# Kernel tuning notes

Measured on AMD Instinct MI355X. Metric: run time of the kernel, lower is better.

## Reference

```python
import jax, jax.numpy as jnp
import numpy as np

N_NODES = 100000
N_EDGES = 3200000
EMBED_DIM = 64
BATCH = 16384


def setup_inputs() -> dict:
    key = jax.random.key(0)
    k1, k2, k3, k4 = jax.random.split(key, 4)
    gcn_weight = jax.random.normal(k1, (N_NODES, EMBED_DIM), dtype=jnp.float32) * 0.1
    gcn_bias = jnp.zeros((EMBED_DIM,), dtype=jnp.float32)
    linear_weight = jax.random.normal(k2, (N_NODES, 1), dtype=jnp.float32) * 0.1
    linear_bias = jnp.zeros((1,), dtype=jnp.float32)
    edge_index = jax.random.randint(k3, (2, N_EDGES), 0, N_NODES, dtype=jnp.int64)
    interaction_pairs = jax.random.randint(k4, (BATCH, 2), 0, N_NODES, dtype=jnp.int64)
    return {
        "gcn_weight": gcn_weight,
        "gcn_bias": gcn_bias,
        "linear_weight": linear_weight,
        "linear_bias": linear_bias,
        "edge_index": edge_index,
        "interaction_pairs": interaction_pairs,
    }


def _gcn_conv_identity_features(gcn_weight, gcn_bias, edge_index):
    # Features X = I, so X @ W = W. GCNConv output = D^{-1/2}(A+I)D^{-1/2} W + b.
    src, dst = edge_index[0], edge_index[1]
    ones = jnp.ones((src.shape[0],), dtype=gcn_weight.dtype)
    # degree (with self loop) computed on destination nodes, as in PyG gcn_norm
    deg = jax.ops.segment_sum(ones, dst, num_segments=N_NODES) + 1.0
    dinv = jax.lax.rsqrt(deg)  # [N]
    norm = dinv[src] * dinv[dst]  # [E]
    msg = gcn_weight[src] * norm[:, None]  # [E, D] -- dominant memory traffic
    agg = jax.ops.segment_sum(msg, dst, num_segments=N_NODES)  # [N, D]
    # self-loop term: norm_ii = 1/deg[i]
    out = agg + gcn_weight * (dinv * dinv)[:, None] + gcn_bias
    return out


def reference(gcn_weight, gcn_bias, linear_weight, linear_bias, edge_index, interaction_pairs):
    node_emb = _gcn_conv_identity_features(gcn_weight, gcn_bias, edge_index)  # [N, D]
    e = node_emb[interaction_pairs]  # [B, 2, D] gather
    # FM pairwise interaction: 0.5 * sum_d ((sum_f e)^2 - sum_f e^2)
    sum_sq = jnp.square(jnp.sum(e, axis=1))  # [B, D]
    sq_sum = jnp.sum(jnp.square(e), axis=1)  # [B, D]
    fm = 0.5 * jnp.sum(sum_sq - sq_sum, axis=1, keepdims=True)  # [B, 1]
    # FeaturesLinear: sum of per-node scalar embeddings + bias
    lin = jnp.sum(linear_weight[interaction_pairs], axis=1) + linear_bias  # [B, 1]
    return jnp.squeeze(lin + fm, axis=1)  # [B]
```

## Files before the change

### kernel.cpp

```cpp
#include <hip/hip_runtime.h>

#define N_NODES 100000
#define N_EDGES 3200000
#define BATCH 16384
#define MAX_SLOTS 32768

#define NW 12500
#define SLICES 256
#define EPS2 12500
#define I4PS2 3125

#define NBUCK 256
#define BCAP 8192
#define BCAP_SH 13
#define EBCAP 4608

#define OFF_SLOT      0
#define OFF_DINV      400000
#define OFF_NODELIST  800000
#define OFF_GCUR      931072
#define OFF_PARTIALS  932096
#define OFF_WH        13732096
#define OFF_BINS      26532096
#define OFF_EMB       34920704

__device__ __forceinline__ unsigned bfr(float f) {
    unsigned u = __float_as_uint(f);
    return (u + 0x7FFFu + ((u >> 16) & 1u)) >> 16;
}
__device__ __forceinline__ float bfx(unsigned h) {
    return __uint_as_float(h << 16);
}

__global__ void k_flags(const int* __restrict__ pairs, unsigned* __restrict__ slot,
                        int* __restrict__ nodelist, unsigned* __restrict__ gcur) {
    int i = blockIdx.x * blockDim.x + threadIdx.x;
    if (i < NBUCK) gcur[i] = (unsigned)(i << BCAP_SH);
    if (i < 2 * BATCH) {
        int n = pairs[i];
        nodelist[i] = n;
        slot[n] = (unsigned)(i + 1);
    }
}

__device__ __forceinline__ int cert(int d, const unsigned* __restrict__ slot,
                                    const int* __restrict__ nodelist) {
    unsigned r = slot[d];
    unsigned idx = r - 1u;
    if (idx < (unsigned)MAX_SLOTS && nodelist[idx] == d) return (int)idx;
    return -1;
}

__global__ void k_hist(const int* __restrict__ src, const int* __restrict__ dst,
                       const unsigned* __restrict__ slot, const int* __restrict__ nodelist,
                       unsigned* __restrict__ partials, unsigned* __restrict__ gcur,
                       unsigned* __restrict__ bins) {
    __shared__ unsigned h[NW];
    __shared__ unsigned ebuf[EBCAP];
    __shared__ int lc[NBUCK];
    __shared__ int base[NBUCK];
    __shared__ int ecnt;
    int g = blockIdx.x;
    int tid = threadIdx.x;
    int lane = tid & 63;
    for (int i = tid; i < NW; i += 512) h[i] = 0;
    if (tid < NBUCK) lc[tid] = 0;
    if (tid == 0) ecnt = 0;
    __syncthreads();
    const int4* d4 = (const int4*)(dst + g * EPS2);
    const int4* s4 = (const int4*)(src + g * EPS2);
    for (int i = tid; i < I4PS2; i += 512) {
        int4 v = d4[i];
        int4 s = s4[i];
        atomicAdd(&h[v.x >> 3], 1u << ((v.x & 7) << 2));
        atomicAdd(&h[v.y >> 3], 1u << ((v.y & 7) << 2));
        atomicAdd(&h[v.z >> 3], 1u << ((v.z & 7) << 2));
        atomicAdd(&h[v.w >> 3], 1u << ((v.w & 7) << 2));
#define STAGE(dc, sc)                                                          \
        {                                                                      \
            int t = cert(dc, slot, nodelist);                                  \
            unsigned long long mk = __ballot(t >= 0);                          \
            int bs = 0;                                                        \
            if (lane == 0) bs = atomicAdd(&ecnt, (int)__popcll(mk));           \
            bs = __shfl(bs, 0, 64);                                            \
            if (t >= 0) {                                                      \
                int off = bs + (int)__popcll(mk & ((1ull << lane) - 1ull));    \
                if (off < EBCAP) {                                             \
                    ebuf[off] = ((unsigned)t << 17) | (unsigned)(sc);          \
                    atomicAdd(&lc[t >> 7], 1);                                 \
                }                                                              \
            }                                                                  \
        }
        STAGE(v.x, s.x)
        STAGE(v.y, s.y)
        STAGE(v.z, s.z)
        STAGE(v.w, s.w)
#undef STAGE
    }
    __syncthreads();
    unsigned* outp = partials + (unsigned)g * NW;
    for (int i = tid; i < NW; i += 512) outp[i] = h[i];
    if (tid < NBUCK) {
        base[tid] = (int)atomicAdd(&gcur[tid], (unsigned)lc[tid]);
        lc[tid] = 0;
    }
    __syncthreads();
    int ne = ecnt;
    if (ne > EBCAP) ne = EBCAP;
    for (int j = tid; j < ne; j += 512) {
        unsigned e = ebuf[j];
        int b = (int)(e >> 24);
        int r = atomicAdd(&lc[b], 1);
        unsigned pos = (unsigned)base[b] + (unsigned)r;
        if (pos < (unsigned)((b + 1) << BCAP_SH)) bins[pos] = e;
    }
}

__global__ void k_mid(const unsigned* __restrict__ partials, const float4* __restrict__ w4,
                      float* __restrict__ dinv, uint4* __restrict__ wh4) {
    __shared__ unsigned pA[256], pB[256], pC[256], pD[256];
    __shared__ float sdinv[256];
    int blk = blockIdx.x;
    int wi = threadIdx.x & 31, sg = threadIdx.x >> 5;
    int w = blk * 32 + wi;
    unsigned A = 0, B = 0, C = 0, D = 0;
    if (w < NW) {
        const unsigned* q = partials + w;
#pragma unroll
        for (int ch = 0; ch < 2; ++ch) {
            unsigned x = 0, y = 0;
#pragma unroll
            for (int k = 0; k < 16; ++k) {
                unsigned v = q[(unsigned)(sg * 32 + ch * 16 + k) * NW];
                x += v & 0x0F0F0F0Fu;
                y += (v >> 4) & 0x0F0F0F0Fu;
            }
            A += x & 0x00FF00FFu;
            B += (x >> 8) & 0x00FF00FFu;
            C += y & 0x00FF00FFu;
            D += (y >> 8) & 0x00FF00FFu;
        }
    }
    pA[threadIdx.x] = A; pB[threadIdx.x] = B; pC[threadIdx.x] = C; pD[threadIdx.x] = D;
    __syncthreads();
    if (threadIdx.x < 32 && w < NW) {
        unsigned sA = 0, sB = 0, sC = 0, sD = 0;
#pragma unroll
        for (int k = 0; k < 8; ++k) {
            sA += pA[k * 32 + wi]; sB += pB[k * 32 + wi];
            sC += pC[k * 32 + wi]; sD += pD[k * 32 + wi];
        }
        float4 d0, d1;
        d0.x = rsqrtf((float)(sA & 0xFFFFu) + 1.0f);
        d0.y = rsqrtf((float)(sC & 0xFFFFu) + 1.0f);
        d0.z = rsqrtf((float)(sB & 0xFFFFu) + 1.0f);
        d0.w = rsqrtf((float)(sD & 0xFFFFu) + 1.0f);
        d1.x = rsqrtf((float)(sA >> 16) + 1.0f);
        d1.y = rsqrtf((float)(sC >> 16) + 1.0f);
        d1.z = rsqrtf((float)(sB >> 16) + 1.0f);
        d1.w = rsqrtf((float)(sD >> 16) + 1.0f);
        ((float4*)dinv)[w * 2] = d0;
        ((float4*)dinv)[w * 2 + 1] = d1;
        int lb = wi * 8;
        sdinv[lb + 0] = d0.x; sdinv[lb + 1] = d0.y; sdinv[lb + 2] = d0.z; sdinv[lb + 3] = d0.w;
        sdinv[lb + 4] = d1.x; sdinv[lb + 5] = d1.y; sdinv[lb + 6] = d1.z; sdinv[lb + 7] = d1.w;
    }
    __syncthreads();
#pragma unroll
    for (int it = 0; it < 8; ++it) {
        int k = blk * 2048 + it * 256 + threadIdx.x;
        if (k < N_NODES * 8) {
            float4 va = w4[k * 2];
            float4 vb = w4[k * 2 + 1];
            float d = sdinv[(k >> 3) - blk * 256];
            uint4 o;
            o.x = bfr(va.x * d) | (bfr(va.y * d) << 16);
            o.y = bfr(va.z * d) | (bfr(va.w * d) << 16);
            o.z = bfr(vb.x * d) | (bfr(vb.y * d) << 16);
            o.w = bfr(vb.z * d) | (bfr(vb.w * d) << 16);
            wh4[k] = o;
        }
    }
}

__global__ void k_gfuse(const unsigned* __restrict__ gcur, const unsigned* __restrict__ bins,
                        const int* __restrict__ nodelist, const uint4* __restrict__ wh4,
                        const float* __restrict__ dinv, const float4* __restrict__ bias4,
                        uint4* __restrict__ emb4) {
    __shared__ unsigned ebuf2[BCAP];
    __shared__ int lc[128], st[128];
    int b = blockIdx.x >> 2;
    int qt = blockIdx.x & 3;
    int tid = threadIdx.x;
    int cnt = (int)(gcur[b] - (unsigned)(b << BCAP_SH));
    if (cnt > BCAP) cnt = BCAP;
    const unsigned* bp = bins + ((unsigned)b << BCAP_SH);
    if (tid < 128) lc[tid] = 0;
    __syncthreads();
    for (int j = tid; j < cnt; j += 512) atomicAdd(&lc[(bp[j] >> 17) & 127], 1);
    __syncthreads();
    if (tid < 128) st[tid] = lc[tid];
    __syncthreads();
    for (int off = 1; off < 128; off <<= 1) {
        int v = (tid < 128 && tid >= off) ? st[tid - off] : 0;
        __syncthreads();
        if (tid < 128) st[tid] += v;
        __syncthreads();
    }
    if (tid < 128) {
        st[tid] -= lc[tid];
        lc[tid] = st[tid];
    }
    __syncthreads();
    for (int j = tid; j < cnt; j += 512) {
        unsigned e = bp[j];
        int r = atomicAdd(&lc[(e >> 17) & 127], 1);
        ebuf2[r] = e & 0x1FFFFu;
    }
    __syncthreads();
    int wave = tid >> 6, lane = tid & 63;
    int rg = lane >> 3, dp = lane & 7;
#pragma unroll
    for (int q = 0; q < 4; ++q) {
        int sl = qt * 32 + wave * 4 + q;
        int s0 = st[sl];
        int cn = lc[sl] - s0;
        double a0 = 0., a1 = 0., a2 = 0., a3 = 0., a4 = 0., a5 = 0., a6 = 0., a7 = 0.;
        int j = 0;
        for (; j + 16 <= cn; j += 16) {
            int e0 = (int)ebuf2[s0 + j + rg];
            int e1 = (int)ebuf2[s0 + j + 8 + rg];
            uint4 oa = wh4[(e0 << 3) + dp];
            uint4 ob = wh4[(e1 << 3) + dp];
            a0 += (double)(bfx(oa.x) + bfx(ob.x));
            a1 += (double)(bfx(oa.x >> 16) + bfx(ob.x >> 16));
            a2 += (double)(bfx(oa.y) + bfx(ob.y));
            a3 += (double)(bfx(oa.y >> 16) + bfx(ob.y >> 16));
            a4 += (double)(bfx(oa.z) + bfx(ob.z));
            a5 += (double)(bfx(oa.z >> 16) + bfx(ob.z >> 16));
            a6 += (double)(bfx(oa.w) + bfx(ob.w));
            a7 += (double)(bfx(oa.w >> 16) + bfx(ob.w >> 16));
        }
        for (; j < cn; j += 8) {
            if (rg < cn - j) {
                int e0 = (int)ebuf2[s0 + j + rg];
                uint4 oa = wh4[(e0 << 3) + dp];
                a0 += (double)bfx(oa.x); a1 += (double)bfx(oa.x >> 16);
                a2 += (double)bfx(oa.y); a3 += (double)bfx(oa.y >> 16);
                a4 += (double)bfx(oa.z); a5 += (double)bfx(oa.z >> 16);
                a6 += (double)bfx(oa.w); a7 += (double)bfx(oa.w >> 16);
            }
        }
#pragma unroll
        for (int m = 8; m <= 32; m <<= 1) {
            a0 += __shfl_xor(a0, m, 64); a1 += __shfl_xor(a1, m, 64);
            a2 += __shfl_xor(a2, m, 64); a3 += __shfl_xor(a3, m, 64);
            a4 += __shfl_xor(a4, m, 64); a5 += __shfl_xor(a5, m, 64);
            a6 += __shfl_xor(a6, m, 64); a7 += __shfl_xor(a7, m, 64);
        }
        if (rg == 0) {
            int gslot = (b << 7) + sl;
            int n = nodelist[gslot];
            float dn = dinv[n];
            uint4 u = wh4[(n << 3) + dp];
            float4 b0 = bias4[dp * 2], b1 = bias4[dp * 2 + 1];
            float r0 = ((float)a0 + bfx(u.x)) * dn + b0.x;
            float r1 = ((float)a1 + bfx(u.x >> 16)) * dn + b0.y;
            float r2 = ((float)a2 + bfx(u.y)) * dn + b0.z;
            float r3 = ((float)a3 + bfx(u.y >> 16)) * dn + b0.w;
            float r4 = ((float)a4 + bfx(u.z)) * dn + b1.x;
            float r5 = ((float)a5 + bfx(u.z >> 16)) * dn + b1.y;
            float r6 = ((float)a6 + bfx(u.w)) * dn + b1.z;
            float r7 = ((float)a7 + bfx(u.w >> 16)) * dn + b1.w;
            uint4 o;
            o.x = bfr(r0) | (bfr(r1) << 16);
            o.y = bfr(r2) | (bfr(r3) << 16);
            o.z = bfr(r4) | (bfr(r5) << 16);
            o.w = bfr(r6) | (bfr(r7) << 16);
            emb4[(gslot << 3) + dp] = o;
        }
    }
}

__global__ void k_final(const int* __restrict__ pairs, const unsigned* __restrict__ slot,
                        const uint2* __restrict__ emb2, const float* __restrict__ lw,
                        const float* __restrict__ lb, float* __restrict__ out) {
    int p = (blockIdx.x * blockDim.x + threadIdx.x) >> 4;
    int li = threadIdx.x & 15;
    if (p >= BATCH) return;
    int a = pairs[p * 2], b = pairs[p * 2 + 1];
    int sa = (int)slot[a] - 1;
    int sb = (int)slot[b] - 1;
    uint2 ua = emb2[(sa << 4) + li];
    uint2 ub = emb2[(sb << 4) + li];
    float prod = bfx(ua.x) * bfx(ub.x) + bfx(ua.x >> 16) * bfx(ub.x >> 16)
               + bfx(ua.y) * bfx(ub.y) + bfx(ua.y >> 16) * bfx(ub.y >> 16);
#pragma unroll
    for (int m = 1; m <= 8; m <<= 1) prod += __shfl_xor(prod, m, 64);
    if (li == 0) out[p] = lw[a] + lw[b] + lb[0] + prod;
}

extern "C" void kernel_launch(void* const* d_in, const int* in_sizes, int n_in,
                              void* d_out, int out_size, void* d_ws, size_t ws_size,
                              hipStream_t stream) {
    const float* gcn_weight    = (const float*)d_in[0];
    const float* gcn_bias      = (const float*)d_in[1];
    const float* linear_weight = (const float*)d_in[2];
    const float* linear_bias   = (const float*)d_in[3];
    const int*   edge_index    = (const int*)d_in[4];
    const int*   pairs         = (const int*)d_in[5];
    float* out = (float*)d_out;

    char* ws = (char*)d_ws;
    unsigned* slot      = (unsigned*)(ws + OFF_SLOT);
    float*    dinv      = (float*)   (ws + OFF_DINV);
    int*      nodelist  = (int*)     (ws + OFF_NODELIST);
    unsigned* gcur      = (unsigned*)(ws + OFF_GCUR);
    unsigned* partials  = (unsigned*)(ws + OFF_PARTIALS);
    uint4*    wh4       = (uint4*)   (ws + OFF_WH);
    unsigned* bins      = (unsigned*)(ws + OFF_BINS);
    uint4*    emb4      = (uint4*)   (ws + OFF_EMB);
    uint2*    emb2      = (uint2*)   (ws + OFF_EMB);

    const int* src_arr = edge_index;
    const int* dst_arr = edge_index + N_EDGES;

    k_flags<<<64, 512, 0, stream>>>(pairs, slot, nodelist, gcur);
    k_hist<<<SLICES, 512, 0, stream>>>(src_arr, dst_arr, slot, nodelist,
                                       partials, gcur, bins);
    k_mid<<<391, 256, 0, stream>>>(partials, (const float4*)gcn_weight, dinv, wh4);
    k_gfuse<<<NBUCK * 4, 512, 0, stream>>>(gcur, bins, nodelist, wh4,
                                           dinv, (const float4*)gcn_bias, emb4);
    k_final<<<1024, 256, 0, stream>>>(pairs, slot, emb2, linear_weight, linear_bias, out);
}
```

Measured before the change: 163.1 us.

## Fuse pipeline into single cooperative kernel with grid-wide syncs

Replaces the five separate kernel launches with one cooperative kernel of 256 blocks that uses grid.sync between phases. The bf16 conversion of the weights moves into the histogram phase, and source-node dinv scaling is applied per edge during aggregation rather than folded into the bf16 weights beforehand. The goal is to remove launch gaps and overlap the weight conversion with the histogram work. In exchange it adds grid barriers and an extra dinv gather per edge, and cuts the gather phase to 256 blocks from the earlier 1024.

```diff
diff --git a/kernel.cpp b/kernel.cpp
--- a/kernel.cpp
+++ b/kernel.cpp
@@ -1,4 +1,7 @@
 #include <hip/hip_runtime.h>
+#include <hip/hip_cooperative_groups.h>
+
+namespace cg = cooperative_groups;
 
 #define N_NODES 100000
 #define N_EDGES 3200000
@@ -14,6 +17,10 @@
 #define BCAP 8192
 #define BCAP_SH 13
 #define EBCAP 4608
+
+#define NTHREADS 512
+#define NBLOCKS 256
+#define GSIZE (NTHREADS * NBLOCKS)
 
 #define OFF_SLOT      0
 #define OFF_DINV      400000
@@ -32,17 +39,6 @@
     return __uint_as_float(h << 16);
 }
 
-__global__ void k_flags(const int* __restrict__ pairs, unsigned* __restrict__ slot,
-                        int* __restrict__ nodelist, unsigned* __restrict__ gcur) {
-    int i = blockIdx.x * blockDim.x + threadIdx.x;
-    if (i < NBUCK) gcur[i] = (unsigned)(i << BCAP_SH);
-    if (i < 2 * BATCH) {
-        int n = pairs[i];
-        nodelist[i] = n;
-        slot[n] = (unsigned)(i + 1);
-    }
-}
-
 __device__ __forceinline__ int cert(int d, const unsigned* __restrict__ slot,
                                     const int* __restrict__ nodelist) {
     unsigned r = slot[d];
@@ -51,253 +47,273 @@
     return -1;
 }
 
-__global__ void k_hist(const int* __restrict__ src, const int* __restrict__ dst,
-                       const unsigned* __restrict__ slot, const int* __restrict__ nodelist,
-                       unsigned* __restrict__ partials, unsigned* __restrict__ gcur,
-                       unsigned* __restrict__ bins) {
-    __shared__ unsigned h[NW];
-    __shared__ unsigned ebuf[EBCAP];
-    __shared__ int lc[NBUCK];
-    __shared__ int base[NBUCK];
-    __shared__ int ecnt;
-    int g = blockIdx.x;
-    int tid = threadIdx.x;
-    int lane = tid & 63;
-    for (int i = tid; i < NW; i += 512) h[i] = 0;
-    if (tid < NBUCK) lc[tid] = 0;
-    if (tid == 0) ecnt = 0;
-    __syncthreads();
-    const int4* d4 = (const int4*)(dst + g * EPS2);
-    const int4* s4 = (const int4*)(src + g * EPS2);
-    for (int i = tid; i < I4PS2; i += 512) {
-        int4 v = d4[i];
-        int4 s = s4[i];
-        atomicAdd(&h[v.x >> 3], 1u << ((v.x & 7) << 2));
-        atomicAdd(&h[v.y >> 3], 1u << ((v.y & 7) << 2));
-        atomicAdd(&h[v.z >> 3], 1u << ((v.z & 7) << 2));
-        atomicAdd(&h[v.w >> 3], 1u << ((v.w & 7) << 2));
+union SharedU {
+    struct { unsigned h[NW]; unsigned ebuf[EBCAP]; int lc[NBUCK]; int base[NBUCK]; int ecnt; } p1;
+    struct { unsigned pA[NTHREADS], pB[NTHREADS], pC[NTHREADS], pD[NTHREADS]; } p2;
+    struct { unsigned ebuf2[BCAP]; int lc[128]; int st[128]; } p3;
+};
+
+__global__ void __launch_bounds__(NTHREADS, 1)
+k_mega(const int* __restrict__ pairs, unsigned* __restrict__ slot,
+       int* __restrict__ nodelist, unsigned* __restrict__ gcur,
+       const int* __restrict__ src, const int* __restrict__ dst,
+       unsigned* __restrict__ partials, unsigned* __restrict__ bins,
+       const float4* __restrict__ w4, float* __restrict__ dinv,
+       uint4* __restrict__ wh4, const float4* __restrict__ bias4,
+       uint4* __restrict__ emb4, const float* __restrict__ lw,
+       const float* __restrict__ lb, float* __restrict__ out) {
+    __shared__ SharedU su;
+    cg::grid_group grid = cg::this_grid();
+    const int tid = threadIdx.x;
+    const int gtid = blockIdx.x * NTHREADS + tid;
+    const int lane = tid & 63;
+
+    if (gtid < NBUCK) gcur[gtid] = (unsigned)(gtid << BCAP_SH);
+    if (gtid < 2 * BATCH) {
+        int n = pairs[gtid];
+        nodelist[gtid] = n;
+        slot[n] = (unsigned)(gtid + 1);
+    }
+    __threadfence();
+    grid.sync();
+
+    {
+        int g = blockIdx.x;
+        for (int i = tid; i < NW; i += NTHREADS) su.p1.h[i] = 0;
+        if (tid < NBUCK) su.p1.lc[tid] = 0;
+        if (tid == 0) su.p1.ecnt = 0;
+        __syncthreads();
+        const int4* d4 = (const int4*)(dst + g * EPS2);
+        const int4* s4 = (const int4*)(src + g * EPS2);
+        for (int i = tid; i < I4PS2; i += NTHREADS) {
+            int4 v = d4[i];
+            int4 s = s4[i];
+            atomicAdd(&su.p1.h[v.x >> 3], 1u << ((v.x & 7) << 2));
+            atomicAdd(&su.p1.h[v.y >> 3], 1u << ((v.y & 7) << 2));
+            atomicAdd(&su.p1.h[v.z >> 3], 1u << ((v.z & 7) << 2));
+            atomicAdd(&su.p1.h[v.w >> 3], 1u << ((v.w & 7) << 2));
 #define STAGE(dc, sc)                                                          \
-        {                                                                      \
-            int t = cert(dc, slot, nodelist);                                  \
-            unsigned long long mk = __ballot(t >= 0);                          \
-            int bs = 0;                                                        \
-            if (lane == 0) bs = atomicAdd(&ecnt, (int)__popcll(mk));           \
-            bs = __shfl(bs, 0, 64);                                            \
-            if (t >= 0) {                                                      \
-                int off = bs + (int)__popcll(mk & ((1ull << lane) - 1ull));    \
-                if (off < EBCAP) {                                             \
-                    ebuf[off] = ((unsigned)t << 17) | (unsigned)(sc);          \
-                    atomicAdd(&lc[t >> 7], 1);                                 \
+            {                                                                  \
+                int t = cert(dc, slot, nodelist);                              \
+                unsigned long long mk = __ballot(t >= 0);                      \
+                int bs = 0;                                                    \
+                if (lane == 0) bs = atomicAdd(&su.p1.ecnt, (int)__popcll(mk)); \
+                bs = __shfl(bs, 0, 64);                                        \
+                if (t >= 0) {                                                  \
+                    int off = bs + (int)__popcll(mk & ((1ull << lane) - 1ull));\
+                    if (off < EBCAP) {                                         \
+                        su.p1.ebuf[off] = ((unsigned)t << 17) | (unsigned)(sc);\
+                        atomicAdd(&su.p1.lc[t >> 7], 1);                       \
+                    }                                                          \
                 }                                                              \
-            }                                                                  \
-        }
-        STAGE(v.x, s.x)
-        STAGE(v.y, s.y)
-        STAGE(v.z, s.z)
-        STAGE(v.w, s.w)
+            }
+            STAGE(v.x, s.x)
+            STAGE(v.y, s.y)
+            STAGE(v.z, s.z)
+            STAGE(v.w, s.w)
 #undef STAGE
-    }
-    __syncthreads();
-    unsigned* outp = partials + (unsigned)g * NW;
-    for (int i = tid; i < NW; i += 512) outp[i] = h[i];
-    if (tid < NBUCK) {
-        base[tid] = (int)atomicAdd(&gcur[tid], (unsigned)lc[tid]);
-        lc[tid] = 0;
-    }
-    __syncthreads();
-    int ne = ecnt;
-    if (ne > EBCAP) ne = EBCAP;
-    for (int j = tid; j < ne; j += 512) {
-        unsigned e = ebuf[j];
-        int b = (int)(e >> 24);
-        int r = atomicAdd(&lc[b], 1);
-        unsigned pos = (unsigned)base[b] + (unsigned)r;
-        if (pos < (unsigned)((b + 1) << BCAP_SH)) bins[pos] = e;
-    }
-}
-
-__global__ void k_mid(const unsigned* __restrict__ partials, const float4* __restrict__ w4,
-                      float* __restrict__ dinv, uint4* __restrict__ wh4) {
-    __shared__ unsigned pA[256], pB[256], pC[256], pD[256];
-    __shared__ float sdinv[256];
-    int blk = blockIdx.x;
-    int wi = threadIdx.x & 31, sg = threadIdx.x >> 5;
-    int w = blk * 32 + wi;
-    unsigned A = 0, B = 0, C = 0, D = 0;
-    if (w < NW) {
-        const unsigned* q = partials + w;
-#pragma unroll
-        for (int ch = 0; ch < 2; ++ch) {
-            unsigned x = 0, y = 0;
-#pragma unroll
-            for (int k = 0; k < 16; ++k) {
-                unsigned v = q[(unsigned)(sg * 32 + ch * 16 + k) * NW];
-                x += v & 0x0F0F0F0Fu;
-                y += (v >> 4) & 0x0F0F0F0Fu;
-            }
-            A += x & 0x00FF00FFu;
-            B += (x >> 8) & 0x00FF00FFu;
-            C += y & 0x00FF00FFu;
-            D += (y >> 8) & 0x00FF00FFu;
-        }
-    }
-    pA[threadIdx.x] = A; pB[threadIdx.x] = B; pC[threadIdx.x] = C; pD[threadIdx.x] = D;
-    __syncthreads();
-    if (threadIdx.x < 32 && w < NW) {
-        unsigned sA = 0, sB = 0, sC = 0, sD = 0;
-#pragma unroll
-        for (int k = 0; k < 8; ++k) {
-            sA += pA[k * 32 + wi]; sB += pB[k * 32 + wi];
-            sC += pC[k * 32 + wi]; sD += pD[k * 32 + wi];
-        }
-        float4 d0, d1;
-        d0.x = rsqrtf((float)(sA & 0xFFFFu) + 1.0f);
-        d0.y = rsqrtf((float)(sC & 0xFFFFu) + 1.0f);
-        d0.z = rsqrtf((float)(sB & 0xFFFFu) + 1.0f);
-        d0.w = rsqrtf((float)(sD & 0xFFFFu) + 1.0f);
-        d1.x = rsqrtf((float)(sA >> 16) + 1.0f);
-        d1.y = rsqrtf((float)(sC >> 16) + 1.0f);
-        d1.z = rsqrtf((float)(sB >> 16) + 1.0f);
-        d1.w = rsqrtf((float)(sD >> 16) + 1.0f);
-        ((float4*)dinv)[w * 2] = d0;
-        ((float4*)dinv)[w * 2 + 1] = d1;
-        int lb = wi * 8;
-        sdinv[lb + 0] = d0.x; sdinv[lb + 1] = d0.y; sdinv[lb + 2] = d0.z; sdinv[lb + 3] = d0.w;
-        sdinv[lb + 4] = d1.x; sdinv[lb + 5] = d1.y; sdinv[lb + 6] = d1.z; sdinv[lb + 7] = d1.w;
-    }
-    __syncthreads();
-#pragma unroll
-    for (int it = 0; it < 8; ++it) {
-        int k = blk * 2048 + it * 256 + threadIdx.x;
-        if (k < N_NODES * 8) {
+        }
+        __syncthreads();
+        unsigned* outp = partials + (unsigned)g * NW;
+        for (int i = tid; i < NW; i += NTHREADS) outp[i] = su.p1.h[i];
+        if (tid < NBUCK) {
+            su.p1.base[tid] = (int)atomicAdd(&gcur[tid], (unsigned)su.p1.lc[tid]);
+            su.p1.lc[tid] = 0;
+        }
+        __syncthreads();
+        int ne = su.p1.ecnt;
+        if (ne > EBCAP) ne = EBCAP;
+        for (int j = tid; j < ne; j += NTHREADS) {
+            unsigned e = su.p1.ebuf[j];
+            int b = (int)(e >> 24);
+            int r = atomicAdd(&su.p1.lc[b], 1);
+            unsigned pos = (unsigned)su.p1.base[b] + (unsigned)r;
+            if (pos < (unsigned)((b + 1) << BCAP_SH)) bins[pos] = e;
+        }
+        for (int k = gtid; k < N_NODES * 8; k += GSIZE) {
             float4 va = w4[k * 2];
             float4 vb = w4[k * 2 + 1];
-            float d = sdinv[(k >> 3) - blk * 256];
             uint4 o;
-            o.x = bfr(va.x * d) | (bfr(va.y * d) << 16);
-            o.y = bfr(va.z * d) | (bfr(va.w * d) << 16);
-            o.z = bfr(vb.x * d) | (bfr(vb.y * d) << 16);
-            o.w = bfr(vb.z * d) | (bfr(vb.w * d) << 16);
+            o.x = bfr(va.x) | (bfr(va.y) << 16);
+            o.y = bfr(va.z) | (bfr(va.w) << 16);
+            o.z = bfr(vb.x) | (bfr(vb.y) << 16);
+            o.w = bfr(vb.z) | (bfr(vb.w) << 16);
             wh4[k] = o;
         }
     }
-}
-
-__global__ void k_gfuse(const unsigned* __restrict__ gcur, const unsigned* __restrict__ bins,
-                        const int* __restrict__ nodelist, const uint4* __restrict__ wh4,
-                        const float* __restrict__ dinv, const float4* __restrict__ bias4,
-                        uint4* __restrict__ emb4) {
-    __shared__ unsigned ebuf2[BCAP];
-    __shared__ int lc[128], st[128];
-    int b = blockIdx.x >> 2;
-    int qt = blockIdx.x & 3;
-    int tid = threadIdx.x;
-    int cnt = (int)(gcur[b] - (unsigned)(b << BCAP_SH));
-    if (cnt > BCAP) cnt = BCAP;
-    const unsigned* bp = bins + ((unsigned)b << BCAP_SH);
-    if (tid < 128) lc[tid] = 0;
-    __syncthreads();
-    for (int j = tid; j < cnt; j += 512) atomicAdd(&lc[(bp[j] >> 17) & 127], 1);
-    __syncthreads();
-    if (tid < 128) st[tid] = lc[tid];
-    __syncthreads();
-    for (int off = 1; off < 128; off <<= 1) {
-        int v = (tid < 128 && tid >= off) ? st[tid - off] : 0;
-        __syncthreads();
-        if (tid < 128) st[tid] += v;
-        __syncthreads();
-    }
-    if (tid < 128) {
-        st[tid] -= lc[tid];
-        lc[tid] = st[tid];
-    }
-    __syncthreads();
-    for (int j = tid; j < cnt; j += 512) {
-        unsigned e = bp[j];
-        int r = atomicAdd(&lc[(e >> 17) & 127], 1);
-        ebuf2[r] = e & 0x1FFFFu;
-    }
-    __syncthreads();
-    int wave = tid >> 6, lane = tid & 63;
-    int rg = lane >> 3, dp = lane & 7;
-#pragma unroll
-    for (int q = 0; q < 4; ++q) {
-        int sl = qt * 32 + wave * 4 + q;
-        int s0 = st[sl];
-        int cn = lc[sl] - s0;
-        double a0 = 0., a1 = 0., a2 = 0., a3 = 0., a4 = 0., a5 = 0., a6 = 0., a7 = 0.;
-        int j = 0;
-        for (; j + 16 <= cn; j += 16) {
-            int e0 = (int)ebuf2[s0 + j + rg];
-            int e1 = (int)ebuf2[s0 + j + 8 + rg];
-            uint4 oa = wh4[(e0 << 3) + dp];
-            uint4 ob = wh4[(e1 << 3) + dp];
-            a0 += (double)(bfx(oa.x) + bfx(ob.x));
-            a1 += (double)(bfx(oa.x >> 16) + bfx(ob.x >> 16));
-            a2 += (double)(bfx(oa.y) + bfx(ob.y));
-            a3 += (double)(bfx(oa.y >> 16) + bfx(ob.y >> 16));
-            a4 += (double)(bfx(oa.z) + bfx(ob.z));
-            a5 += (double)(bfx(oa.z >> 16) + bfx(ob.z >> 16));
-            a6 += (double)(bfx(oa.w) + bfx(ob.w));
-            a7 += (double)(bfx(oa.w >> 16) + bfx(ob.w >> 16));
-        }
-        for (; j < cn; j += 8) {
-            if (rg < cn - j) {
-                int e0 = (int)ebuf2[s0 + j + rg];
+    __threadfence();
+    grid.sync();
+
+    {
+        int vb = blockIdx.x;
+        if (vb < 196) {
+            int wi = tid & 63, sg = tid >> 6;
+            int w = vb * 64 + wi;
+            unsigned A = 0, B = 0, C = 0, D = 0;
+            if (w < NW) {
+                const unsigned* q = partials + w;
+#pragma unroll
+                for (int ch = 0; ch < 2; ++ch) {
+                    unsigned x = 0, y = 0;
+#pragma unroll
+                    for (int k = 0; k < 16; ++k) {
+                        unsigned v = q[(unsigned)(sg * 32 + ch * 16 + k) * NW];
+                        x += v & 0x0F0F0F0Fu;
+                        y += (v >> 4) & 0x0F0F0F0Fu;
+                    }
+                    A += x & 0x00FF00FFu;
+                    B += (x >> 8) & 0x00FF00FFu;
+                    C += y & 0x00FF00FFu;
+                    D += (y >> 8) & 0x00FF00FFu;
+                }
+            }
+            su.p2.pA[tid] = A; su.p2.pB[tid] = B; su.p2.pC[tid] = C; su.p2.pD[tid] = D;
+            __syncthreads();
+            if (tid < 64 && w < NW) {
+                unsigned sA = 0, sB = 0, sC = 0, sD = 0;
+#pragma unroll
+                for (int k = 0; k < 8; ++k) {
+                    sA += su.p2.pA[k * 64 + tid]; sB += su.p2.pB[k * 64 + tid];
+                    sC += su.p2.pC[k * 64 + tid]; sD += su.p2.pD[k * 64 + tid];
+                }
+                float4 d0, d1;
+                d0.x = rsqrtf((float)(sA & 0xFFFFu) + 1.0f);
+                d0.y = rsqrtf((float)(sC & 0xFFFFu) + 1.0f);
+                d0.z = rsqrtf((float)(sB & 0xFFFFu) + 1.0f);
+                d0.w = rsqrtf((float)(sD & 0xFFFFu) + 1.0f);
+                d1.x = rsqrtf((float)(sA >> 16) + 1.0f);
+                d1.y = rsqrtf((float)(sC >> 16) + 1.0f);
+                d1.z = rsqrtf((float)(sB >> 16) + 1.0f);
+                d1.w = rsqrtf((float)(sD >> 16) + 1.0f);
+                ((float4*)dinv)[w * 2] = d0;
+                ((float4*)dinv)[w * 2 + 1] = d1;
+            }
+        }
+    }
+    __threadfence();
+    grid.sync();
+
+    {
+        int b = blockIdx.x;
+        int cnt = (int)(gcur[b] - (unsigned)(b << BCAP_SH));
+        if (cnt > BCAP) cnt = BCAP;
+        const unsigned* bp = bins + ((unsigned)b << BCAP_SH);
+        if (tid < 128) su.p3.lc[tid] = 0;
+        __syncthreads();
+        for (int j = tid; j < cnt; j += NTHREADS)
+            atomicAdd(&su.p3.lc[(bp[j] >> 17) & 127], 1);
+        __syncthreads();
+        if (tid < 128) su.p3.st[tid] = su.p3.lc[tid];
+        __syncthreads();
+        for (int off = 1; off < 128; off <<= 1) {
+            int v = (tid < 128 && tid >= off) ? su.p3.st[tid - off] : 0;
+            __syncthreads();
+            if (tid < 128) su.p3.st[tid] += v;
+            __syncthreads();
+        }
+        if (tid < 128) {
+            su.p3.st[tid] -= su.p3.lc[tid];
+            su.p3.lc[tid] = su.p3.st[tid];
+        }
+        __syncthreads();
+        for (int j = tid; j < cnt; j += NTHREADS) {
+            unsigned e = bp[j];
+            int r = atomicAdd(&su.p3.lc[(e >> 17) & 127], 1);
+            su.p3.ebuf2[r] = e & 0x1FFFFu;
+        }
+        __syncthreads();
+        int wave = tid >> 6;
+        int rg = lane >> 3, dp = lane & 7;
+#pragma unroll 1
+        for (int q = 0; q < 16; ++q) {
+            int sl = wave * 16 + q;
+            int s0 = su.p3.st[sl];
+            int cn = su.p3.lc[sl] - s0;
+            double a0 = 0., a1 = 0., a2 = 0., a3 = 0., a4 = 0., a5 = 0., a6 = 0., a7 = 0.;
+            int j = 0;
+            for (; j + 16 <= cn; j += 16) {
+                int e0 = (int)su.p3.ebuf2[s0 + j + rg];
+                int e1 = (int)su.p3.ebuf2[s0 + j + 8 + rg];
+                float dv0 = dinv[e0], dv1 = dinv[e1];
                 uint4 oa = wh4[(e0 << 3) + dp];
-                a0 += (double)bfx(oa.x); a1 += (double)bfx(oa.x >> 16);
-                a2 += (double)bfx(oa.y); a3 += (double)bfx(oa.y >> 16);
-                a4 += (double)bfx(oa.z); a5 += (double)bfx(oa.z >> 16);
-                a6 += (double)bfx(oa.w); a7 += (double)bfx(oa.w >> 16);
-            }
-        }
-#pragma unroll
-        for (int m = 8; m <= 32; m <<= 1) {
-            a0 += __shfl_xor(a0, m, 64); a1 += __shfl_xor(a1, m, 64);
-            a2 += __shfl_xor(a2, m, 64); a3 += __shfl_xor(a3, m, 64);
-            a4 += __shfl_xor(a4, m, 64); a5 += __shfl_xor(a5, m, 64);
-            a6 += __shfl_xor(a6, m, 64); a7 += __shfl_xor(a7, m, 64);
-        }
-        if (rg == 0) {
-            int gslot = (b << 7) + sl;
-            int n = nodelist[gslot];
-            float dn = dinv[n];
-            uint4 u = wh4[(n << 3) + dp];
-            float4 b0 = bias4[dp * 2], b1 = bias4[dp * 2 + 1];
-            float r0 = ((float)a0 + bfx(u.x)) * dn + b0.x;
-            float r1 = ((float)a1 + bfx(u.x >> 16)) * dn + b0.y;
-            float r2 = ((float)a2 + bfx(u.y)) * dn + b0.z;
-            float r3 = ((float)a3 + bfx(u.y >> 16)) * dn + b0.w;
-            float r4 = ((float)a4 + bfx(u.z)) * dn + b1.x;
-            float r5 = ((float)a5 + bfx(u.z >> 16)) * dn + b1.y;
-            float r6 = ((float)a6 + bfx(u.w)) * dn + b1.z;
-            float r7 = ((float)a7 + bfx(u.w >> 16)) * dn + b1.w;
-            uint4 o;
-            o.x = bfr(r0) | (bfr(r1) << 16);
-            o.y = bfr(r2) | (bfr(r3) << 16);
-            o.z = bfr(r4) | (bfr(r5) << 16);
-            o.w = bfr(r6) | (bfr(r7) << 16);
-            emb4[(gslot << 3) + dp] = o;
-        }
-    }
-}
-
-__global__ void k_final(const int* __restrict__ pairs, const unsigned* __restrict__ slot,
-                        const uint2* __restrict__ emb2, const float* __restrict__ lw,
-                        const float* __restrict__ lb, float* __restrict__ out) {
-    int p = (blockIdx.x * blockDim.x + threadIdx.x) >> 4;
-    int li = threadIdx.x & 15;
-    if (p >= BATCH) return;
-    int a = pairs[p * 2], b = pairs[p * 2 + 1];
-    int sa = (int)slot[a] - 1;
-    int sb = (int)slot[b] - 1;
-    uint2 ua = emb2[(sa << 4) + li];
-    uint2 ub = emb2[(sb << 4) + li];
-    float prod = bfx(ua.x) * bfx(ub.x) + bfx(ua.x >> 16) * bfx(ub.x >> 16)
-               + bfx(ua.y) * bfx(ub.y) + bfx(ua.y >> 16) * bfx(ub.y >> 16);
-#pragma unroll
-    for (int m = 1; m <= 8; m <<= 1) prod += __shfl_xor(prod, m, 64);
-    if (li == 0) out[p] = lw[a] + lw[b] + lb[0] + prod;
+                uint4 ob = wh4[(e1 << 3) + dp];
+                a0 += (double)(bfx(oa.x) * dv0 + bfx(ob.x) * dv1);
+                a1 += (double)(bfx(oa.x >> 16) * dv0 + bfx(ob.x >> 16) * dv1);
+                a2 += (double)(bfx(oa.y) * dv0 + bfx(ob.y) * dv1);
+                a3 += (double)(bfx(oa.y >> 16) * dv0 + bfx(ob.y >> 16) * dv1);
+                a4 += (double)(bfx(oa.z) * dv0 + bfx(ob.z) * dv1);
+                a5 += (double)(bfx(oa.z >> 16) * dv0 + bfx(ob.z >> 16) * dv1);
+                a6 += (double)(bfx(oa.w) * dv0 + bfx(ob.w) * dv1);
+                a7 += (double)(bfx(oa.w >> 16) * dv0 + bfx(ob.w >> 16) * dv1);
+            }
+            for (; j < cn; j += 8) {
+                if (rg < cn - j) {
+                    int e0 = (int)su.p3.ebuf2[s0 + j + rg];
+                    float dv0 = dinv[e0];
+                    uint4 oa = wh4[(e0 << 3) + dp];
+                    a0 += (double)(bfx(oa.x) * dv0);
+                    a1 += (double)(bfx(oa.x >> 16) * dv0);
+                    a2 += (double)(bfx(oa.y) * dv0);
+                    a3 += (double)(bfx(oa.y >> 16) * dv0);
+                    a4 += (double)(bfx(oa.z) * dv0);
+                    a5 += (double)(bfx(oa.z >> 16) * dv0);
+                    a6 += (double)(bfx(oa.w) * dv0);
+                    a7 += (double)(bfx(oa.w >> 16) * dv0);
+                }
+            }
+#pragma unroll
+            for (int m = 8; m <= 32; m <<= 1) {
+                a0 += __shfl_xor(a0, m, 64); a1 += __shfl_xor(a1, m, 64);
+                a2 += __shfl_xor(a2, m, 64); a3 += __shfl_xor(a3, m, 64);
+                a4 += __shfl_xor(a4, m, 64); a5 += __shfl_xor(a5, m, 64);
+                a6 += __shfl_xor(a6, m, 64); a7 += __shfl_xor(a7, m, 64);
+            }
+            if (rg == 0) {
+                int gslot = (b << 7) + sl;
+                int n = nodelist[gslot];
+                float dn = dinv[n];
+                uint4 u = wh4[(n << 3) + dp];
+                float4 b0 = bias4[dp * 2], b1 = bias4[dp * 2 + 1];
+                float r0 = ((float)a0 + bfx(u.x) * dn) * dn + b0.x;
+                float r1 = ((float)a1 + bfx(u.x >> 16) * dn) * dn + b0.y;
+                float r2 = ((float)a2 + bfx(u.y) * dn) * dn + b0.z;
+                float r3 = ((float)a3 + bfx(u.y >> 16) * dn) * dn + b0.w;
+                float r4 = ((float)a4 + bfx(u.z) * dn) * dn + b1.x;
+                float r5 = ((float)a5 + bfx(u.z >> 16) * dn) * dn + b1.y;
+                float r6 = ((float)a6 + bfx(u.w) * dn) * dn + b1.z;
+                float r7 = ((float)a7 + bfx(u.w >> 16) * dn) * dn + b1.w;
+                uint4 o;
+                o.x = bfr(r0) | (bfr(r1) << 16);
+                o.y = bfr(r2) | (bfr(r3) << 16);
+                o.z = bfr(r4) | (bfr(r5) << 16);
+                o.w = bfr(r6) | (bfr(r7) << 16);
+                emb4[(gslot << 3) + dp] = o;
+            }
+        }
+    }
+    __threadfence();
+    grid.sync();
+
+    {
+        const uint2* emb2 = (const uint2*)emb4;
+        int li = tid & 15;
+#pragma unroll
+        for (int pass = 0; pass < 2; ++pass) {
+            int p = pass * (GSIZE / 16) + (gtid >> 4);
+            if (p < BATCH) {
+                int a = pairs[p * 2], b = pairs[p * 2 + 1];
+                int sa = (int)slot[a] - 1;
+                int sb = (int)slot[b] - 1;
+                uint2 ua = emb2[(sa << 4) + li];
+                uint2 ub = emb2[(sb << 4) + li];
+                float prod = bfx(ua.x) * bfx(ub.x) + bfx(ua.x >> 16) * bfx(ub.x >> 16)
+                           + bfx(ua.y) * bfx(ub.y) + bfx(ua.y >> 16) * bfx(ub.y >> 16);
+#pragma unroll
+                for (int m = 1; m <= 8; m <<= 1) prod += __shfl_xor(prod, m, 64);
+                if (li == 0) out[p] = lw[a] + lw[b] + lb[0] + prod;
+            }
+        }
+    }
 }
 
 extern "C" void kernel_launch(void* const* d_in, const int* in_sizes, int n_in,
@@ -308,7 +324,7 @@
     const float* linear_weight = (const float*)d_in[2];
     const float* linear_bias   = (const float*)d_in[3];
     const int*   edge_index    = (const int*)d_in[4];
-    const int*   pairs         = (const int*)d_in[5];
+    const int*   pairs_p       = (const int*)d_in[5];
     float* out = (float*)d_out;
 
     char* ws = (char*)d_ws;
@@ -320,16 +336,18 @@
     uint4*    wh4       = (uint4*)   (ws + OFF_WH);
     unsigned* bins      = (unsigned*)(ws + OFF_BINS);
     uint4*    emb4      = (uint4*)   (ws + OFF_EMB);
-    uint2*    emb2      = (uint2*)   (ws + OFF_EMB);
 
     const int* src_arr = edge_index;
     const int* dst_arr = edge_index + N_EDGES;
-
-    k_flags<<<64, 512, 0, stream>>>(pairs, slot, nodelist, gcur);
-    k_hist<<<SLICES, 512, 0, stream>>>(src_arr, dst_arr, slot, nodelist,
-                                       partials, gcur, bins);
-    k_mid<<<391, 256, 0, stream>>>(partials, (const float4*)gcn_weight, dinv, wh4);
-    k_gfuse<<<NBUCK * 4, 512, 0, stream>>>(gcur, bins, nodelist, wh4,
-                                           dinv, (const float4*)gcn_bias, emb4);
-    k_final<<<1024, 256, 0, stream>>>(pairs, slot, emb2, linear_weight, linear_bias, out);
-}
+    const float4* w4f   = (const float4*)gcn_weight;
+    const float4* bias4 = (const float4*)gcn_bias;
+
+    void* args[] = {
+        (void*)&pairs_p, (void*)&slot, (void*)&nodelist, (void*)&gcur,
+        (void*)&src_arr, (void*)&dst_arr, (void*)&partials, (void*)&bins,
+        (void*)&w4f, (void*)&dinv, (void*)&wh4, (void*)&bias4,
+        (void*)&emb4, (void*)&linear_weight, (void*)&linear_bias, (void*)&out
+    };
+    hipLaunchCooperativeKernel((const void*)k_mega, dim3(NBLOCKS), dim3(NTHREADS),
+                               args, 0, stream);
+}
```

Result: slower. 497.6 us (+205.0%).

## Move bf16 weight conversion into histogram kernel and apply dinv at gather

Applied to the files above, without the earlier changes.

The fp32-to-bf16 conversion of the GCN weight table moves out of k_mid and into the tail of k_hist, with no dinv scaling applied there. The gather kernel now loads dinv[src] per edge and multiplies it in, and applies dn to the self-loop term as well. This leaves k_mid as a small degree-reduction kernel. k_hist and k_gfuse move to 1024-thread blocks, and k_gfuse uses half as many blocks with its q loop no longer unrolled. The cost is an extra random 4-byte dinv load per edge in the gather, and the conversion now sits on k_hist's critical path.

```diff
diff --git a/kernel.cpp b/kernel.cpp
--- a/kernel.cpp
+++ b/kernel.cpp
@@ -14,6 +14,9 @@
 #define BCAP 8192
 #define BCAP_SH 13
 #define EBCAP 4608
+
+#define HIST_THREADS 1024
+#define HGSIZE (SLICES * HIST_THREADS)
 
 #define OFF_SLOT      0
 #define OFF_DINV      400000
@@ -54,7 +57,8 @@
 __global__ void k_hist(const int* __restrict__ src, const int* __restrict__ dst,
                        const unsigned* __restrict__ slot, const int* __restrict__ nodelist,
                        unsigned* __restrict__ partials, unsigned* __restrict__ gcur,
-                       unsigned* __restrict__ bins) {
+                       unsigned* __restrict__ bins,
+                       const float4* __restrict__ w4, uint4* __restrict__ wh4) {
     __shared__ unsigned h[NW];
     __shared__ unsigned ebuf[EBCAP];
     __shared__ int lc[NBUCK];
@@ -63,13 +67,13 @@
     int g = blockIdx.x;
     int tid = threadIdx.x;
     int lane = tid & 63;
-    for (int i = tid; i < NW; i += 512) h[i] = 0;
+    for (int i = tid; i < NW; i += HIST_THREADS) h[i] = 0;
     if (tid < NBUCK) lc[tid] = 0;
     if (tid == 0) ecnt = 0;
     __syncthreads();
     const int4* d4 = (const int4*)(dst + g * EPS2);
     const int4* s4 = (const int4*)(src + g * EPS2);
-    for (int i = tid; i < I4PS2; i += 512) {
+    for (int i = tid; i < I4PS2; i += HIST_THREADS) {
         int4 v = d4[i];
         int4 s = s4[i];
         atomicAdd(&h[v.x >> 3], 1u << ((v.x & 7) << 2));
@@ -99,7 +103,7 @@
     }
     __syncthreads();
     unsigned* outp = partials + (unsigned)g * NW;
-    for (int i = tid; i < NW; i += 512) outp[i] = h[i];
+    for (int i = tid; i < NW; i += HIST_THREADS) outp[i] = h[i];
     if (tid < NBUCK) {
         base[tid] = (int)atomicAdd(&gcur[tid], (unsigned)lc[tid]);
         lc[tid] = 0;
@@ -107,19 +111,27 @@
     __syncthreads();
     int ne = ecnt;
     if (ne > EBCAP) ne = EBCAP;
-    for (int j = tid; j < ne; j += 512) {
+    for (int j = tid; j < ne; j += HIST_THREADS) {
         unsigned e = ebuf[j];
         int b = (int)(e >> 24);
         int r = atomicAdd(&lc[b], 1);
         unsigned pos = (unsigned)base[b] + (unsigned)r;
         if (pos < (unsigned)((b + 1) << BCAP_SH)) bins[pos] = e;
     }
-}
-
-__global__ void k_mid(const unsigned* __restrict__ partials, const float4* __restrict__ w4,
-                      float* __restrict__ dinv, uint4* __restrict__ wh4) {
+    for (int k = g * HIST_THREADS + tid; k < N_NODES * 8; k += HGSIZE) {
+        float4 va = w4[k * 2];
+        float4 vb = w4[k * 2 + 1];
+        uint4 o;
+        o.x = bfr(va.x) | (bfr(va.y) << 16);
+        o.y = bfr(va.z) | (bfr(va.w) << 16);
+        o.z = bfr(vb.x) | (bfr(vb.y) << 16);
+        o.w = bfr(vb.z) | (bfr(vb.w) << 16);
+        wh4[k] = o;
+    }
+}
+
+__global__ void k_mid(const unsigned* __restrict__ partials, float* __restrict__ dinv) {
     __shared__ unsigned pA[256], pB[256], pC[256], pD[256];
-    __shared__ float sdinv[256];
     int blk = blockIdx.x;
     int wi = threadIdx.x & 31, sg = threadIdx.x >> 5;
     int w = blk * 32 + wi;
@@ -161,25 +173,6 @@
         d1.w = rsqrtf((float)(sD >> 16) + 1.0f);
         ((float4*)dinv)[w * 2] = d0;
         ((float4*)dinv)[w * 2 + 1] = d1;
-        int lb = wi * 8;
-        sdinv[lb + 0] = d0.x; sdinv[lb + 1] = d0.y; sdinv[lb + 2] = d0.z; sdinv[lb + 3] = d0.w;
-        sdinv[lb + 4] = d1.x; sdinv[lb + 5] = d1.y; sdinv[lb + 6] = d1.z; sdinv[lb + 7] = d1.w;
-    }
-    __syncthreads();
-#pragma unroll
-    for (int it = 0; it < 8; ++it) {
-        int k = blk * 2048 + it * 256 + threadIdx.x;
-        if (k < N_NODES * 8) {
-            float4 va = w4[k * 2];
-            float4 vb = w4[k * 2 + 1];
-            float d = sdinv[(k >> 3) - blk * 256];
-            uint4 o;
-            o.x = bfr(va.x * d) | (bfr(va.y * d) << 16);
-            o.y = bfr(va.z * d) | (bfr(va.w * d) << 16);
-            o.z = bfr(vb.x * d) | (bfr(vb.y * d) << 16);
-            o.w = bfr(vb.z * d) | (bfr(vb.w * d) << 16);
-            wh4[k] = o;
-        }
     }
 }
 
@@ -189,15 +182,15 @@
                         uint4* __restrict__ emb4) {
     __shared__ unsigned ebuf2[BCAP];
     __shared__ int lc[128], st[128];
-    int b = blockIdx.x >> 2;
-    int qt = blockIdx.x & 3;
+    int b = blockIdx.x >> 1;
+    int half = blockIdx.x & 1;
     int tid = threadIdx.x;
     int cnt = (int)(gcur[b] - (unsigned)(b << BCAP_SH));
     if (cnt > BCAP) cnt = BCAP;
     const unsigned* bp = bins + ((unsigned)b << BCAP_SH);
     if (tid < 128) lc[tid] = 0;
     __syncthreads();
-    for (int j = tid; j < cnt; j += 512) atomicAdd(&lc[(bp[j] >> 17) & 127], 1);
+    for (int j = tid; j < cnt; j += 1024) atomicAdd(&lc[(bp[j] >> 17) & 127], 1);
     __syncthreads();
     if (tid < 128) st[tid] = lc[tid];
     __syncthreads();
@@ -212,7 +205,7 @@
         lc[tid] = st[tid];
     }
     __syncthreads();
-    for (int j = tid; j < cnt; j += 512) {
+    for (int j = tid; j < cnt; j += 1024) {
         unsigned e = bp[j];
         int r = atomicAdd(&lc[(e >> 17) & 127], 1);
         ebuf2[r] = e & 0x1FFFFu;
@@ -220,9 +213,9 @@
     __syncthreads();
     int wave = tid >> 6, lane = tid & 63;
     int rg = lane >> 3, dp = lane & 7;
-#pragma unroll
+#pragma unroll 1
     for (int q = 0; q < 4; ++q) {
-        int sl = qt * 32 + wave * 4 + q;
+        int sl = half * 64 + wave * 4 + q;
         int s0 = st[sl];
         int cn = lc[sl] - s0;
         double a0 = 0., a1 = 0., a2 = 0., a3 = 0., a4 = 0., a5 = 0., a6 = 0., a7 = 0.;
@@ -230,25 +223,31 @@
         for (; j + 16 <= cn; j += 16) {
             int e0 = (int)ebuf2[s0 + j + rg];
             int e1 = (int)ebuf2[s0 + j + 8 + rg];
+            float dv0 = dinv[e0], dv1 = dinv[e1];
             uint4 oa = wh4[(e0 << 3) + dp];
             uint4 ob = wh4[(e1 << 3) + dp];
-            a0 += (double)(bfx(oa.x) + bfx(ob.x));
-            a1 += (double)(bfx(oa.x >> 16) + bfx(ob.x >> 16));
-            a2 += (double)(bfx(oa.y) + bfx(ob.y));
-            a3 += (double)(bfx(oa.y >> 16) + bfx(ob.y >> 16));
-            a4 += (double)(bfx(oa.z) + bfx(ob.z));
-            a5 += (double)(bfx(oa.z >> 16) + bfx(ob.z >> 16));
-            a6 += (double)(bfx(oa.w) + bfx(ob.w));
-            a7 += (double)(bfx(oa.w >> 16) + bfx(ob.w >> 16));
+            a0 += (double)(bfx(oa.x) * dv0 + bfx(ob.x) * dv1);
+            a1 += (double)(bfx(oa.x >> 16) * dv0 + bfx(ob.x >> 16) * dv1);
+            a2 += (double)(bfx(oa.y) * dv0 + bfx(ob.y) * dv1);
+            a3 += (double)(bfx(oa.y >> 16) * dv0 + bfx(ob.y >> 16) * dv1);
+            a4 += (double)(bfx(oa.z) * dv0 + bfx(ob.z) * dv1);
+            a5 += (double)(bfx(oa.z >> 16) * dv0 + bfx(ob.z >> 16) * dv1);
+            a6 += (double)(bfx(oa.w) * dv0 + bfx(ob.w) * dv1);
+            a7 += (double)(bfx(oa.w >> 16) * dv0 + bfx(ob.w >> 16) * dv1);
         }
         for (; j < cn; j += 8) {
             if (rg < cn - j) {
                 int e0 = (int)ebuf2[s0 + j + rg];
+                float dv0 = dinv[e0];
                 uint4 oa = wh4[(e0 << 3) + dp];
-                a0 += (double)bfx(oa.x); a1 += (double)bfx(oa.x >> 16);
-                a2 += (double)bfx(oa.y); a3 += (double)bfx(oa.y >> 16);
-                a4 += (double)bfx(oa.z); a5 += (double)bfx(oa.z >> 16);
-                a6 += (double)bfx(oa.w); a7 += (double)bfx(oa.w >> 16);
+                a0 += (double)(bfx(oa.x) * dv0);
+                a1 += (double)(bfx(oa.x >> 16) * dv0);
+                a2 += (double)(bfx(oa.y) * dv0);
+                a3 += (double)(bfx(oa.y >> 16) * dv0);
+                a4 += (double)(bfx(oa.z) * dv0);
+                a5 += (double)(bfx(oa.z >> 16) * dv0);
+                a6 += (double)(bfx(oa.w) * dv0);
+                a7 += (double)(bfx(oa.w >> 16) * dv0);
             }
         }
 #pragma unroll
@@ -264,14 +263,14 @@
             float dn = dinv[n];
             uint4 u = wh4[(n << 3) + dp];
             float4 b0 = bias4[dp * 2], b1 = bias4[dp * 2 + 1];
-            float r0 = ((float)a0 + bfx(u.x)) * dn + b0.x;
-            float r1 = ((float)a1 + bfx(u.x >> 16)) * dn + b0.y;
-            float r2 = ((float)a2 + bfx(u.y)) * dn + b0.z;
-            float r3 = ((float)a3 + bfx(u.y >> 16)) * dn + b0.w;
-            float r4 = ((float)a4 + bfx(u.z)) * dn + b1.x;
-            float r5 = ((float)a5 + bfx(u.z >> 16)) * dn + b1.y;
-            float r6 = ((float)a6 + bfx(u.w)) * dn + b1.z;
-            float r7 = ((float)a7 + bfx(u.w >> 16)) * dn + b1.w;
+            float r0 = ((float)a0 + bfx(u.x) * dn) * dn + b0.x;
+            float r1 = ((float)a1 + bfx(u.x >> 16) * dn) * dn + b0.y;
+            float r2 = ((float)a2 + bfx(u.y) * dn) * dn + b0.z;
+            float r3 = ((float)a3 + bfx(u.y >> 16) * dn) * dn + b0.w;
+            float r4 = ((float)a4 + bfx(u.z) * dn) * dn + b1.x;
+            float r5 = ((float)a5 + bfx(u.z >> 16) * dn) * dn + b1.y;
+            float r6 = ((float)a6 + bfx(u.w) * dn) * dn + b1.z;
+            float r7 = ((float)a7 + bfx(u.w >> 16) * dn) * dn + b1.w;
             uint4 o;
             o.x = bfr(r0) | (bfr(r1) << 16);
             o.y = bfr(r2) | (bfr(r3) << 16);
@@ -326,10 +325,11 @@
     const int* dst_arr = edge_index + N_EDGES;
 
     k_flags<<<64, 512, 0, stream>>>(pairs, slot, nodelist, gcur);
-    k_hist<<<SLICES, 512, 0, stream>>>(src_arr, dst_arr, slot, nodelist,
-                                       partials, gcur, bins);
-    k_mid<<<391, 256, 0, stream>>>(partials, (const float4*)gcn_weight, dinv, wh4);
-    k_gfuse<<<NBUCK * 4, 512, 0, stream>>>(gcur, bins, nodelist, wh4,
-                                           dinv, (const float4*)gcn_bias, emb4);
+    k_hist<<<SLICES, HIST_THREADS, 0, stream>>>(src_arr, dst_arr, slot, nodelist,
+                                                partials, gcur, bins,
+                                                (const float4*)gcn_weight, wh4);
+    k_mid<<<391, 256, 0, stream>>>(partials, dinv);
+    k_gfuse<<<NBUCK * 2, 1024, 0, stream>>>(gcur, bins, nodelist, wh4,
+                                            dinv, (const float4*)gcn_bias, emb4);
     k_final<<<1024, 256, 0, stream>>>(pairs, slot, emb2, linear_weight, linear_bias, out);
 }
```

After: 158.7 us. -2.7%, faster.
